# Kernel optimization log

Hardware: AMD Instinct MI355X
Metric: run time of the kernel (lower is better)

Reference implementation:

```python
import jax, jax.numpy as jnp
import numpy as np

D_MODEL = 2048
SLOTS = 8
D_FIELD = 256  # SLOTS * D_FIELD == proj output dim == 2048
BATCH = 2
SEQ = 4096


def setup_inputs() -> dict:
    key = jax.random.key(0)
    k1, k2 = jax.random.split(key, 2)
    x = jax.random.normal(k1, (BATCH, SEQ, D_MODEL), dtype=jnp.float32)
    # nn.Linear(d_model, slots*d_field): weight [out, in], bias [out]
    W = jax.random.normal(k2, (SLOTS * D_FIELD, D_MODEL), dtype=jnp.float32) * (1.0 / np.sqrt(D_MODEL))
    b = jnp.zeros((SLOTS * D_FIELD,), dtype=jnp.float32)
    horizons = jnp.array([1., 2., 4., 8., 16., 32., 64., 128.], dtype=jnp.float32)
    alphas = jnp.exp(-1.0 / horizons)  # per-slot EMA decay, length SLOTS
    return {"x": x, "W": W, "b": b, "alphas": alphas}


def reference(x, W, b, alphas):
    B, S, _ = x.shape
    # projection: [B,S,d_model] @ [d_model, slots*d_field] -> [B,S,slots,d_field]
    updates = (jnp.einsum('bsd,od->bso', x, W) + b).reshape(B, S, SLOTS, D_FIELD)
    # linear recurrence state_t = alpha * state_{t-1} + u_t, state_0 = 0,
    # via log-depth associative scan with elements (a_t, u_t)
    a = jnp.broadcast_to(alphas[None, None, :, None], updates.shape)

    def combine(c1, c2):
        a1, u1 = c1
        a2, u2 = c2
        return (a1 * a2, a2 * u1 + u2)

    _, state = jax.lax.associative_scan(combine, (a, updates), axis=1)
    return state  # [B,S,slots,d_field]
```

## Files before the change

kernel.cpp:

```cpp
#include <hip/hip_runtime.h>
#include <hip/hip_bf16.h>
#include <stdint.h>
#include <stddef.h>

#define D_MODEL 2048
#define NOUT    2048
#define BATCH   2
#define SEQ     4096
#define M_TOTAL (BATCH*SEQ)
#define SLOTS   8
#define D_FIELD 256
#define CHUNK   64
#define NCHUNK  (SEQ/CHUNK)

typedef __attribute__((ext_vector_type(4))) float  floatx4;
typedef __attribute__((ext_vector_type(8))) __bf16 bf16x8;
typedef __attribute__((ext_vector_type(4))) __bf16 bf16x4;

__device__ __forceinline__ void async_copy16(const void* gsrc, void* ldst) {
  __builtin_amdgcn_global_load_lds(
      (__attribute__((address_space(1))) const void*)(uintptr_t)gsrc,
      (__attribute__((address_space(3))) void*)(uintptr_t)ldst,
      16, 0, 0);
}

__global__ void cast_kernel(const float* __restrict__ x,
                            const float* __restrict__ W,
                            __bf16* __restrict__ xb,
                            __bf16* __restrict__ wb) {
  const long long nx = (long long)M_TOTAL * D_MODEL;
  const long long nw = (long long)NOUT * D_MODEL;
  long long base = ((long long)blockIdx.x * blockDim.x + threadIdx.x) * 4;
  if (base < nx) {
    float4 v = *(const float4*)(x + base);
    bf16x4 o;
    o[0] = (__bf16)v.x; o[1] = (__bf16)v.y; o[2] = (__bf16)v.z; o[3] = (__bf16)v.w;
    *(bf16x4*)(xb + base) = o;
  } else {
    long long j = base - nx;
    if (j < nw) {
      float4 v = *(const float4*)(W + j);
      bf16x4 o;
      o[0] = (__bf16)v.x; o[1] = (__bf16)v.y; o[2] = (__bf16)v.z; o[3] = (__bf16)v.w;
      *(bf16x4*)(wb + j) = o;
    }
  }
}

__global__ __launch_bounds__(256) void gemm_scan_kernel(
    const __bf16* __restrict__ A,
    const __bf16* __restrict__ Bw,
    const float*  __restrict__ bias,
    const float*  __restrict__ alphas,
    float* __restrict__ C,
    float* __restrict__ carry) {
  __shared__ __align__(16) __bf16 sA[128 * 64];
  __shared__ __align__(16) __bf16 sB[128 * 64];

  const int t    = threadIdx.x;
  const int lane = t & 63;
  const int wave = t >> 6;
  const int wM   = wave >> 1;
  const int wN   = wave & 1;
  const int m0   = blockIdx.x * 128;
  const int n0   = blockIdx.y * 128;
  const int K    = D_MODEL;

  const int r0 = t >> 3;
  const int g  = (t & 7) ^ (r0 & 7);
  const __bf16* gA = A  + (size_t)(m0 + r0) * K + g * 8;
  const __bf16* gB = Bw + (size_t)(n0 + r0) * K + g * 8;
  __bf16* lA = sA + t * 8;
  __bf16* lB = sB + t * 8;

  const int q = lane >> 4;
  const int L = lane & 15;
  const int xorL = L & 7;
  const __bf16* fA = sA + (wM * 64 + L) * 64;
  const __bf16* fB = sB + (wN * 64 + L) * 64;

  floatx4 acc[4][4] = {};

  for (int kt = 0; kt < K; kt += 64) {
    __syncthreads();
#pragma unroll
    for (int i = 0; i < 4; ++i) {
      async_copy16(gA + kt + (size_t)i * 32 * K, lA + i * 2048);
      async_copy16(gB + kt + (size_t)i * 32 * K, lB + i * 2048);
    }
    __syncthreads();
#pragma unroll
    for (int kk = 0; kk < 2; ++kk) {
      const int slot = (((kk * 4 + q) ^ xorL)) * 8;
      bf16x8 af[4], bfr[4];
#pragma unroll
      for (int mi = 0; mi < 4; ++mi) af[mi]  = *(const bf16x8*)(fA + mi * 1024 + slot);
#pragma unroll
      for (int ni = 0; ni < 4; ++ni) bfr[ni] = *(const bf16x8*)(fB + ni * 1024 + slot);
#pragma unroll
      for (int mi = 0; mi < 4; ++mi)
#pragma unroll
        for (int ni = 0; ni < 4; ++ni)
          acc[mi][ni] = __builtin_amdgcn_mfma_f32_16x16x32_bf16(
              af[mi], bfr[ni], acc[mi][ni], 0, 0, 0);
    }
  }

  const int mBase = m0 + wM * 64 + q * 4;
  const int nBase = n0 + wN * 64 + L;
  const float alpha = alphas[(n0 + wN * 64) >> 8];
  const float a4  = (alpha * alpha) * (alpha * alpha);
  const float a16 = (a4 * a4) * (a4 * a4);
  float aq = 1.f;
#pragma unroll
  for (int i = 0; i < 3; ++i) if (i < 3 - q) aq *= a4;
  const int gm0 = m0 + wM * 64;
  const int bb  = gm0 >> 12;
  const int jj  = (gm0 & (SEQ - 1)) >> 6;

#pragma unroll
  for (int ni = 0; ni < 4; ++ni) {
    const int n = nBase + ni * 16;
    const float bv = bias[n];
    float tmi[4];
#pragma unroll
    for (int mi = 0; mi < 4; ++mi) {
      const int m = mBase + mi * 16;
      float u[4];
#pragma unroll
      for (int r = 0; r < 4; ++r) {
        u[r] = acc[mi][ni][r] + bv;
        C[(size_t)(m + r) * NOUT + n] = u[r];
      }
      tmi[mi] = ((u[0] * alpha + u[1]) * alpha + u[2]) * alpha + u[3];
    }
    float s = ((tmi[0] * a16 + tmi[1]) * a16 + tmi[2]) * a16 + tmi[3];
    s *= aq;
    s += __shfl_xor(s, 16, 64);
    s += __shfl_xor(s, 32, 64);
    if (q == 0)
      carry[(size_t)(bb * NCHUNK + jj) * NOUT + n] = s;
  }
}

__global__ void scan_apply(float* __restrict__ U,
                           const float* __restrict__ alphas,
                           const float* __restrict__ carry) {
  const int idx  = blockIdx.x * blockDim.x + threadIdx.x;
  const int c    = idx & (NOUT - 1);
  const int rest = idx >> 11;
  const int j    = rest & (NCHUNK - 1);
  const int b    = rest >> 6;
  const float alpha = alphas[c >> 8];
  float a64 = alpha;
#pragma unroll
  for (int i = 0; i < 6; ++i) a64 *= a64;

  const float* cb = carry + (size_t)b * NCHUNK * NOUT + c;
  float s = 0.f;
#pragma unroll 8
  for (int jp = 0; jp < j; ++jp)
    s = a64 * s + cb[(size_t)jp * NOUT];

  float* p = U + ((size_t)(b * SEQ + j * CHUNK) * NOUT) + c;
#pragma unroll 8
  for (int tt = 0; tt < CHUNK; ++tt) {
    const float v = alpha * s + p[(size_t)tt * NOUT];
    p[(size_t)tt * NOUT] = v;
    s = v;
  }
}

extern "C" void kernel_launch(void* const* d_in, const int* in_sizes, int n_in,
                              void* d_out, int out_size, void* d_ws, size_t ws_size,
                              hipStream_t stream) {
  const float* x      = (const float*)d_in[0];
  const float* W      = (const float*)d_in[1];
  const float* bias   = (const float*)d_in[2];
  const float* alphas = (const float*)d_in[3];
  float* out = (float*)d_out;

  __bf16* xb   = (__bf16*)d_ws;
  __bf16* wb   = (__bf16*)((char*)d_ws + (size_t)M_TOTAL * D_MODEL * 2);
  float* carry = (float*)((char*)d_ws + (size_t)M_TOTAL * D_MODEL * 2
                                       + (size_t)NOUT * D_MODEL * 2);

  {
    const long long total = ((long long)M_TOTAL * D_MODEL + (long long)NOUT * D_MODEL) / 4;
    const int blocks = (int)((total + 255) / 256);
    cast_kernel<<<blocks, 256, 0, stream>>>(x, W, xb, wb);
  }
  {
    dim3 grid(M_TOTAL / 128, NOUT / 128);
    gemm_scan_kernel<<<grid, 256, 0, stream>>>(xb, wb, bias, alphas, out, carry);
  }
  scan_apply<<<(BATCH * NCHUNK * NOUT) / 256, 256, 0, stream>>>(out, alphas, carry);
}
```

Baseline: 223.0 us.

## Rewrite GEMM as 256x256 double-buffered pipelined tile with 8 waves

The GEMM moves to 256x256 tiles with 512 threads and 128KB of dynamic LDS used as two buffers. Global-to-LDS copies for the next K tile are interleaved with the MFMA quarters, using explicit vmcnt waits, barriers and setprio, so loads overlap compute instead of running behind full syncs. The scan chunk shrinks to 32 rows so each wave's 128-row slab yields four carries, and scan_apply is adjusted to match. The gain depends on the hand-written schedule and on 128KB LDS fitting; the apply step now runs over twice as many chunks, so its serial carry loop gets longer.

```diff
diff --git a/kernel.cpp b/kernel.cpp
--- a/kernel.cpp
+++ b/kernel.cpp
@@ -10,8 +10,9 @@
 #define M_TOTAL (BATCH*SEQ)
 #define SLOTS   8
 #define D_FIELD 256
-#define CHUNK   64
+#define CHUNK   32
 #define NCHUNK  (SEQ/CHUNK)
+#define NT      (D_MODEL/64)
 
 typedef __attribute__((ext_vector_type(4))) float  floatx4;
 typedef __attribute__((ext_vector_type(8))) __bf16 bf16x8;
@@ -47,99 +48,155 @@
   }
 }
 
-__global__ __launch_bounds__(256) void gemm_scan_kernel(
+#define VMW4 asm volatile("s_waitcnt vmcnt(4)" ::: "memory")
+#define VMW2 asm volatile("s_waitcnt vmcnt(2)" ::: "memory")
+#define VMW0 asm volatile("s_waitcnt vmcnt(0)" ::: "memory")
+#define LGKM0 do{ asm volatile("s_waitcnt lgkmcnt(0)" ::: "memory"); \
+                  __builtin_amdgcn_sched_barrier(0); }while(0)
+#define BAR do{ __builtin_amdgcn_s_barrier(); __builtin_amdgcn_sched_barrier(0); }while(0)
+
+#define DSRD(off) (*(const bf16x8*)(smem + (off)))
+
+#define STG(GP, ROFF, DSTOFF, KTN) do{ \
+  async_copy16((GP) + (ROFF) + (KTN)*64,      smem + (DSTOFF)); \
+  async_copy16((GP) + (ROFF) + (KTN)*64 + 32, smem + (DSTOFF) + 1024); }while(0)
+
+#define RD_AF(BUF, MOFF) do{ \
+  _Pragma("unroll") for (int i_ = 0; i_ < 4; ++i_){ \
+  _Pragma("unroll") for (int k_ = 0; k_ < 2; ++k_){ \
+    afr[i_][k_] = DSRD((BUF)*32768 + ((wM8+(MOFF)+i_)*2+k_)*1024 + fragOff); }} }while(0)
+
+#define RD_BF(BUF, NOFF, DST) do{ \
+  _Pragma("unroll") for (int j_ = 0; j_ < 2; ++j_){ \
+  _Pragma("unroll") for (int k_ = 0; k_ < 2; ++k_){ \
+    DST[j_][k_] = DSRD(65536 + (BUF)*32768 + ((wN4+(NOFF)+j_)*2+k_)*1024 + fragOff); }} }while(0)
+
+#define MFMA_Q(AM, AN, BFR) do{ \
+  __builtin_amdgcn_s_setprio(1); \
+  _Pragma("unroll") for (int i_ = 0; i_ < 4; ++i_){ \
+  _Pragma("unroll") for (int j_ = 0; j_ < 2; ++j_){ \
+  _Pragma("unroll") for (int k_ = 0; k_ < 2; ++k_){ \
+    acc[(AM)+i_][(AN)+j_] = __builtin_amdgcn_mfma_f32_16x16x32_bf16( \
+        afr[i_][k_], BFR[j_][k_], acc[(AM)+i_][(AN)+j_], 0, 0, 0); }}} \
+  __builtin_amdgcn_s_setprio(0); }while(0)
+
+#define KTILE(BUF, KTN, DO_STG) do{ \
+   \
+  RD_AF(BUF, 0); \
+  RD_BF(BUF, 0, bfr0); \
+  if (DO_STG) STG(gA, rA0, ((BUF)^1)*32768 + dA0, KTN); \
+  if (DO_STG) { VMW4; } else { VMW2; } \
+  BAR; LGKM0; \
+  MFMA_Q(0, 0, bfr0); \
+   \
+  RD_BF(BUF, 2, bfr1); \
+  if (DO_STG) STG(gB, rB0, ((BUF)^1)*32768 + dB0, KTN); \
+  if (DO_STG) { VMW4; } else { VMW0; } \
+  BAR; LGKM0; \
+  MFMA_Q(0, 2, bfr1); \
+   \
+  RD_AF(BUF, 4); \
+  if (DO_STG) STG(gB, rB1, ((BUF)^1)*32768 + dB1, KTN); \
+  BAR; LGKM0; \
+  MFMA_Q(4, 2, bfr1); \
+   \
+  if (DO_STG) { STG(gA, rA1, ((BUF)^1)*32768 + dA1, KTN); VMW4; } \
+  BAR; \
+  MFMA_Q(4, 0, bfr0); \
+}while(0)
+
+__global__ __launch_bounds__(512, 2) void gemm_scan_kernel(
     const __bf16* __restrict__ A,
     const __bf16* __restrict__ Bw,
     const float*  __restrict__ bias,
     const float*  __restrict__ alphas,
     float* __restrict__ C,
     float* __restrict__ carry) {
-  __shared__ __align__(16) __bf16 sA[128 * 64];
-  __shared__ __align__(16) __bf16 sB[128 * 64];
-
+  extern __shared__ __align__(16) char smem[];
   const int t    = threadIdx.x;
   const int lane = t & 63;
-  const int wave = t >> 6;
-  const int wM   = wave >> 1;
-  const int wN   = wave & 1;
-  const int m0   = blockIdx.x * 128;
-  const int n0   = blockIdx.y * 128;
-  const int K    = D_MODEL;
-
-  const int r0 = t >> 3;
-  const int g  = (t & 7) ^ (r0 & 7);
-  const __bf16* gA = A  + (size_t)(m0 + r0) * K + g * 8;
-  const __bf16* gB = Bw + (size_t)(n0 + r0) * K + g * 8;
-  __bf16* lA = sA + t * 8;
-  __bf16* lB = sB + t * 8;
-
-  const int q = lane >> 4;
-  const int L = lane & 15;
-  const int xorL = L & 7;
-  const __bf16* fA = sA + (wM * 64 + L) * 64;
-  const __bf16* fB = sB + (wN * 64 + L) * 64;
-
-  floatx4 acc[4][4] = {};
-
-  for (int kt = 0; kt < K; kt += 64) {
-    __syncthreads();
-#pragma unroll
-    for (int i = 0; i < 4; ++i) {
-      async_copy16(gA + kt + (size_t)i * 32 * K, lA + i * 2048);
-      async_copy16(gB + kt + (size_t)i * 32 * K, lB + i * 2048);
+  const int w    = t >> 6;
+  const int wM   = w >> 2;
+  const int wN   = w & 3;
+  const int m0   = blockIdx.x * 256;
+  const int n0   = blockIdx.y * 256;
+
+  const int lq = lane >> 4, lr = lane & 15;
+  const int fragOff = (lr*64 + lq*16) ^ (((lr >> 3) & 1) << 5);
+  const int wM8 = wM*8, wN4 = wN*4;
+
+  const int lrow = lane >> 2;
+  const int lcol = ((lane & 3) * 8) ^ ((lane >> 5) * 16);
+  const int srA0 = (w & 3) + ((w >> 2) << 3), srA1 = srA0 + 4;
+  const int srB0 = (w & 1) + ((w >> 1) << 2), srB1 = srB0 + 2;
+  const __bf16* gA = A  + (size_t)m0 * D_MODEL + lcol;
+  const __bf16* gB = Bw + (size_t)n0 * D_MODEL + lcol;
+  const int rA0 = (srA0*16 + lrow) * D_MODEL;
+  const int rA1 = (srA1*16 + lrow) * D_MODEL;
+  const int rB0 = (srB0*16 + lrow) * D_MODEL;
+  const int rB1 = (srB1*16 + lrow) * D_MODEL;
+  const int dA0 = srA0*2048 + lane*16;
+  const int dA1 = srA1*2048 + lane*16;
+  const int dB0 = 65536 + srB0*2048 + lane*16;
+  const int dB1 = 65536 + srB1*2048 + lane*16;
+
+  floatx4 acc[8][4] = {};
+  bf16x8 afr[4][2], bfr0[2][2], bfr1[2][2];
+
+  STG(gA, rA0, dA0, 0);
+  STG(gB, rB0, dB0, 0);
+  STG(gB, rB1, dB1, 0);
+  STG(gA, rA1, dA1, 0);
+  VMW4;
+  BAR;
+
+#pragma unroll 1
+  for (int p = 0; p < 15; ++p) {
+    KTILE(0, 2*p+1, true);
+    KTILE(1, 2*p+2, true);
+  }
+  KTILE(0, 31, true);
+  KTILE(1, 0, false);
+
+  const int mW0 = m0 + wM*128;
+  const int nW0 = n0 + wN*64;
+  const float alpha = alphas[nW0 >> 8];
+  const float a2 = alpha*alpha;
+  const float a4 = a2*a2;
+  const float a8 = a4*a4;
+  const float a16 = a8*a8;
+  float aq = 1.f;
+#pragma unroll
+  for (int i = 0; i < 3; ++i) if (i < 3 - lq) aq *= a4;
+  const int bb = mW0 >> 12;
+  const int j0 = (mW0 & (SEQ - 1)) >> 5;
+
+#pragma unroll
+  for (int nf = 0; nf < 4; ++nf) {
+    const int n = nW0 + nf*16 + lr;
+    const float bv = bias[n];
+    float tm[8];
+#pragma unroll
+    for (int mf = 0; mf < 8; ++mf) {
+      const int m = mW0 + mf*16 + lq*4;
+      const float u0 = acc[mf][nf][0] + bv;
+      const float u1 = acc[mf][nf][1] + bv;
+      const float u2 = acc[mf][nf][2] + bv;
+      const float u3 = acc[mf][nf][3] + bv;
+      C[(size_t)(m+0)*NOUT + n] = u0;
+      C[(size_t)(m+1)*NOUT + n] = u1;
+      C[(size_t)(m+2)*NOUT + n] = u2;
+      C[(size_t)(m+3)*NOUT + n] = u3;
+      tm[mf] = ((u0*alpha + u1)*alpha + u2)*alpha + u3;
     }
-    __syncthreads();
-#pragma unroll
-    for (int kk = 0; kk < 2; ++kk) {
-      const int slot = (((kk * 4 + q) ^ xorL)) * 8;
-      bf16x8 af[4], bfr[4];
-#pragma unroll
-      for (int mi = 0; mi < 4; ++mi) af[mi]  = *(const bf16x8*)(fA + mi * 1024 + slot);
-#pragma unroll
-      for (int ni = 0; ni < 4; ++ni) bfr[ni] = *(const bf16x8*)(fB + ni * 1024 + slot);
-#pragma unroll
-      for (int mi = 0; mi < 4; ++mi)
-#pragma unroll
-        for (int ni = 0; ni < 4; ++ni)
-          acc[mi][ni] = __builtin_amdgcn_mfma_f32_16x16x32_bf16(
-              af[mi], bfr[ni], acc[mi][ni], 0, 0, 0);
+#pragma unroll
+    for (int c = 0; c < 4; ++c) {
+      float s = (tm[2*c]*a16 + tm[2*c+1]) * aq;
+      s += __shfl_xor(s, 16, 64);
+      s += __shfl_xor(s, 32, 64);
+      if (lq == 0)
+        carry[((size_t)bb*NCHUNK + j0 + c)*NOUT + n] = s;
     }
-  }
-
-  const int mBase = m0 + wM * 64 + q * 4;
-  const int nBase = n0 + wN * 64 + L;
-  const float alpha = alphas[(n0 + wN * 64) >> 8];
-  const float a4  = (alpha * alpha) * (alpha * alpha);
-  const float a16 = (a4 * a4) * (a4 * a4);
-  float aq = 1.f;
-#pragma unroll
-  for (int i = 0; i < 3; ++i) if (i < 3 - q) aq *= a4;
-  const int gm0 = m0 + wM * 64;
-  const int bb  = gm0 >> 12;
-  const int jj  = (gm0 & (SEQ - 1)) >> 6;
-
-#pragma unroll
-  for (int ni = 0; ni < 4; ++ni) {
-    const int n = nBase + ni * 16;
-    const float bv = bias[n];
-    float tmi[4];
-#pragma unroll
-    for (int mi = 0; mi < 4; ++mi) {
-      const int m = mBase + mi * 16;
-      float u[4];
-#pragma unroll
-      for (int r = 0; r < 4; ++r) {
-        u[r] = acc[mi][ni][r] + bv;
-        C[(size_t)(m + r) * NOUT + n] = u[r];
-      }
-      tmi[mi] = ((u[0] * alpha + u[1]) * alpha + u[2]) * alpha + u[3];
-    }
-    float s = ((tmi[0] * a16 + tmi[1]) * a16 + tmi[2]) * a16 + tmi[3];
-    s *= aq;
-    s += __shfl_xor(s, 16, 64);
-    s += __shfl_xor(s, 32, 64);
-    if (q == 0)
-      carry[(size_t)(bb * NCHUNK + jj) * NOUT + n] = s;
   }
 }
 
@@ -150,17 +207,17 @@
   const int c    = idx & (NOUT - 1);
   const int rest = idx >> 11;
   const int j    = rest & (NCHUNK - 1);
-  const int b    = rest >> 6;
+  const int b    = rest >> 7;
   const float alpha = alphas[c >> 8];
-  float a64 = alpha;
-#pragma unroll
-  for (int i = 0; i < 6; ++i) a64 *= a64;
+  float aC = alpha;
+#pragma unroll
+  for (int i = 0; i < 5; ++i) aC *= aC;
 
   const float* cb = carry + (size_t)b * NCHUNK * NOUT + c;
   float s = 0.f;
 #pragma unroll 8
   for (int jp = 0; jp < j; ++jp)
-    s = a64 * s + cb[(size_t)jp * NOUT];
+    s = aC * s + cb[(size_t)jp * NOUT];
 
   float* p = U + ((size_t)(b * SEQ + j * CHUNK) * NOUT) + c;
 #pragma unroll 8
@@ -191,8 +248,8 @@
     cast_kernel<<<blocks, 256, 0, stream>>>(x, W, xb, wb);
   }
   {
-    dim3 grid(M_TOTAL / 128, NOUT / 128);
-    gemm_scan_kernel<<<grid, 256, 0, stream>>>(xb, wb, bias, alphas, out, carry);
+    dim3 grid(M_TOTAL / 256, NOUT / 256);
+    gemm_scan_kernel<<<grid, 512, 131072, stream>>>(xb, wb, bias, alphas, out, carry);
   }
   scan_apply<<<(BATCH * NCHUNK * NOUT) / 256, 256, 0, stream>>>(out, alphas, carry);
 }
```

After: 211.0 us. 5.4% less time.
